# Kernel tuning notes

Measured on AMD Instinct MI355X. Metric: run time of the kernel, lower is better.

Reference implementation:

```python
import jax, jax.numpy as jnp
import numpy as np

B, S, T, V, E, H = 32, 64, 64, 32000, 512, 1024


def setup_inputs() -> dict:
    key = jax.random.key(0)
    ks = jax.random.split(key, 12)
    n = lambda k, shp, s=0.05: jax.random.normal(k, shp, dtype=jnp.float32) * s
    return {
        "src": jax.random.randint(ks[0], (B, S), 0, V, dtype=jnp.int32),
        "tgt": jax.random.randint(ks[1], (B, T), 0, V, dtype=jnp.int32),
        "enc_emb": n(ks[2], (V, E)),
        "dec_emb": n(ks[3], (V, E)),
        "Wih_e": n(ks[4], (E, H)), "bih_e": jnp.zeros((H,), jnp.float32),
        "Whh_e": n(ks[5], (H, H)), "bhh_e": jnp.zeros((H,), jnp.float32),
        "Wih_d": n(ks[6], (E, H)), "bih_d": jnp.zeros((H,), jnp.float32),
        "Whh_d": n(ks[7], (H, H)), "bhh_d": jnp.zeros((H,), jnp.float32),
        "Wout": n(ks[8], (H, V)), "bout": jnp.zeros((V,), jnp.float32),
    }


def reference(src, tgt, enc_emb, dec_emb, Wih_e, bih_e, Whh_e, bhh_e,
              Wih_d, bih_d, Whh_d, bhh_d, Wout, bout):
    # Embedding lookups: [B, S, E] / [B, T, E]
    src_e = enc_emb[src]
    tgt_e = dec_emb[tgt]
    # Precompute input-to-hidden projections for every timestep (same math,
    # batched into one GEMM each): [B, S, H] / [B, T, H]
    x_e = jnp.einsum('bse,eh->bsh', src_e, Wih_e) + bih_e
    x_d = jnp.einsum('bte,eh->bth', tgt_e, Wih_d) + bih_d

    h0 = jnp.zeros((src.shape[0], Whh_e.shape[0]), dtype=x_e.dtype)

    def enc_step(h, x):  # h,x: [B, H]
        h = jnp.tanh(x + h @ Whh_e + bhh_e)
        return h, None

    h_enc, _ = jax.lax.scan(enc_step, h0, jnp.swapaxes(x_e, 0, 1))

    def dec_step(h, x):
        h = jnp.tanh(x + h @ Whh_d + bhh_d)
        return h, h

    _, hs = jax.lax.scan(dec_step, h_enc, jnp.swapaxes(x_d, 0, 1))  # [T, B, H]

    logits = jnp.einsum('tbh,hv->tbv', hs, Wout) + bout  # [T, B, V]
    out = jax.nn.log_softmax(logits, axis=-1)
    return jnp.swapaxes(out, 0, 1)  # [B, T, V]
```

## Files before the change

### kernel.cpp

```cpp
#include <hip/hip_runtime.h>
#include <hip/hip_bf16.h>
#include <math.h>

#define B_ 32
#define S_ 64
#define T_ 64
#define V_ 32000
#define E_ 512
#define H_ 1024

typedef __attribute__((ext_vector_type(8))) short short8;
typedef __attribute__((ext_vector_type(4))) float f32x4;

static __device__ __forceinline__ unsigned short f2bf(float f) {
  union { float f; unsigned u; } c; c.f = f;
  unsigned r = (c.u + 0x7fffu + ((c.u >> 16) & 1u)) >> 16;
  return (unsigned short)r;
}

__global__ __launch_bounds__(256)
void dgemm_embed(const int* __restrict__ idx, const float* __restrict__ emb,
                 const float* __restrict__ B, const float* __restrict__ bias,
                 float* __restrict__ C, int M, int N, int K) {
  __shared__ float As[32][68];
  __shared__ float Bs[32][64];
  const int nbm = M >> 6;
  const int bm = blockIdx.x % nbm;
  const int bn = blockIdx.x / nbm;
  const int tid = threadIdx.x;
  const int tr = tid >> 4, tc = tid & 15;

  const int arow = tid >> 3, acol = (tid & 7) * 4;
  const float* arp[2];
#pragma unroll
  for (int p = 0; p < 2; ++p) {
    int r = arow + p * 32;
    arp[p] = emb + (size_t)idx[bm * 64 + r] * E_;
  }

  double acc[4][4] = {};

  for (int kt = 0; kt < K; kt += 32) {
    {
#pragma unroll
      for (int p = 0; p < 2; ++p) {
        int r = arow + p * 32;
        float4 v = *(const float4*)(arp[p] + kt + acol);
        As[acol + 0][r] = v.x; As[acol + 1][r] = v.y;
        As[acol + 2][r] = v.z; As[acol + 3][r] = v.w;
      }
      int brow = tid >> 4, bcol = (tid & 15) * 4;
#pragma unroll
      for (int p = 0; p < 2; ++p) {
        int r = brow + p * 16;
        float4 v = *(const float4*)(B + (size_t)(kt + r) * N + bn * 64 + bcol);
        *(float4*)(&Bs[r][bcol]) = v;
      }
    }
    __syncthreads();
#pragma unroll
    for (int k = 0; k < 32; ++k) {
      float4 av = *(const float4*)(&As[k][tr * 4]);
      float4 bv = *(const float4*)(&Bs[k][tc * 4]);
      double a[4] = {(double)av.x, (double)av.y, (double)av.z, (double)av.w};
      double b[4] = {(double)bv.x, (double)bv.y, (double)bv.z, (double)bv.w};
#pragma unroll
      for (int i = 0; i < 4; ++i)
#pragma unroll
        for (int j = 0; j < 4; ++j) acc[i][j] = fma(a[i], b[j], acc[i][j]);
    }
    __syncthreads();
  }
#pragma unroll
  for (int i = 0; i < 4; ++i) {
    int gm = bm * 64 + tr * 4 + i;
    int gn = bn * 64 + tc * 4;
    float4 o;
    o.x = (float)(acc[i][0] + (double)bias[gn + 0]);
    o.y = (float)(acc[i][1] + (double)bias[gn + 1]);
    o.z = (float)(acc[i][2] + (double)bias[gn + 2]);
    o.w = (float)(acc[i][3] + (double)bias[gn + 3]);
    *(float4*)(C + (size_t)gm * N + gn) = o;
  }
}

__global__ __launch_bounds__(256)
void transpose_f32(const float* __restrict__ W, float* __restrict__ WT,
                   int K, int N) {
  __shared__ float t[64][65];
  int k0 = blockIdx.x * 64;
  int n0 = blockIdx.y * 64;
  int tid = threadIdx.x;
  int r = tid >> 4, c4 = tid & 15;
#pragma unroll
  for (int i = 0; i < 4; ++i) {
    int row = r + i * 16;
    float4 v = *(const float4*)(W + (size_t)(k0 + row) * N + n0 + c4 * 4);
    t[row][c4 * 4 + 0] = v.x; t[row][c4 * 4 + 1] = v.y;
    t[row][c4 * 4 + 2] = v.z; t[row][c4 * 4 + 3] = v.w;
  }
  __syncthreads();
#pragma unroll
  for (int i = 0; i < 4; ++i) {
    int n = r + i * 16;
    float4 o;
    o.x = t[c4 * 4 + 0][n]; o.y = t[c4 * 4 + 1][n];
    o.z = t[c4 * 4 + 2][n]; o.w = t[c4 * 4 + 3][n];
    *(float4*)(WT + (size_t)(n0 + n) * K + k0 + c4 * 4) = o;
  }
}

__global__ __launch_bounds__(256)
void transpose_bf16(const float* __restrict__ W, unsigned short* __restrict__ WT,
                    int K, int N) {
  __shared__ float t[64][65];
  int k0 = blockIdx.x * 64;
  int n0 = blockIdx.y * 64;
  int tid = threadIdx.x;
  int r = tid >> 4, c4 = tid & 15;
#pragma unroll
  for (int i = 0; i < 4; ++i) {
    int row = r + i * 16;
    float4 v = *(const float4*)(W + (size_t)(k0 + row) * N + n0 + c4 * 4);
    t[row][c4 * 4 + 0] = v.x; t[row][c4 * 4 + 1] = v.y;
    t[row][c4 * 4 + 2] = v.z; t[row][c4 * 4 + 3] = v.w;
  }
  __syncthreads();
#pragma unroll
  for (int i = 0; i < 4; ++i) {
    int n = r + i * 16;
    ushort4 o;
    o.x = f2bf(t[c4 * 4 + 0][n]); o.y = f2bf(t[c4 * 4 + 1][n]);
    o.z = f2bf(t[c4 * 4 + 2][n]); o.w = f2bf(t[c4 * 4 + 3][n]);
    *(ushort4*)(WT + (size_t)(n0 + n) * K + k0 + c4 * 4) = o;
  }
}

__global__ __launch_bounds__(256)
void gemm_bt_swap(const unsigned short* __restrict__ A, const unsigned short* __restrict__ BT,
                  const float* __restrict__ bias, float* __restrict__ C,
                  int M, int N, int K) {
  __shared__ unsigned short As[128 * 64];
  __shared__ unsigned short Bs[128 * 64];
  const int nbm = M >> 7;
  int idx = blockIdx.x;
  const int cpx = gridDim.x >> 3;
  idx = (idx & 7) * cpx + (idx >> 3);
  const int bm = idx % nbm;
  const int bn = idx / nbm;
  const int tid = threadIdx.x;
  const int lane = tid & 63;
  const int wr = (tid >> 6) >> 1;
  const int wc = (tid >> 6) & 1;

  f32x4 acc[4][4] = {};

  int srow[4], scol8[4], ssw[4];
#pragma unroll
  for (int i = 0; i < 4; ++i) {
    int c = i * 256 + tid;
    srow[i] = c >> 3; scol8[i] = c & 7;
    ssw[i] = scol8[i] ^ (srow[i] & 7);
  }

  short8 av[4], bv[4];
#pragma unroll
  for (int i = 0; i < 4; ++i) {
    av[i] = *(const short8*)(A + (size_t)(bm * 128 + srow[i]) * K + scol8[i] * 8);
    bv[i] = *(const short8*)(BT + (size_t)(bn * 128 + srow[i]) * K + scol8[i] * 8);
  }

  for (int kt = 0; kt < K; kt += 64) {
#pragma unroll
    for (int i = 0; i < 4; ++i) {
      *(short8*)(As + srow[i] * 64 + ssw[i] * 8) = av[i];
      *(short8*)(Bs + srow[i] * 64 + ssw[i] * 8) = bv[i];
    }
    __syncthreads();

    if (kt + 64 < K) {
#pragma unroll
      for (int i = 0; i < 4; ++i) {
        av[i] = *(const short8*)(A + (size_t)(bm * 128 + srow[i]) * K + kt + 64 + scol8[i] * 8);
        bv[i] = *(const short8*)(BT + (size_t)(bn * 128 + srow[i]) * K + kt + 64 + scol8[i] * 8);
      }
    }

#pragma unroll
    for (int kk = 0; kk < 64; kk += 32) {
      int kc = (kk + ((lane >> 4) << 3)) >> 3;
      short8 af[4], bfr[4];
#pragma unroll
      for (int mi = 0; mi < 4; ++mi) {
        int row = wr * 64 + mi * 16 + (lane & 15);
        af[mi] = *(const short8*)(As + row * 64 + ((kc ^ (row & 7)) << 3));
      }
#pragma unroll
      for (int ni = 0; ni < 4; ++ni) {
        int row = wc * 64 + ni * 16 + (lane & 15);
        bfr[ni] = *(const short8*)(Bs + row * 64 + ((kc ^ (row & 7)) << 3));
      }
#pragma unroll
      for (int mi = 0; mi < 4; ++mi)
#pragma unroll
        for (int ni = 0; ni < 4; ++ni)
          acc[mi][ni] = __builtin_amdgcn_mfma_f32_16x16x32_bf16(
              af[mi], bfr[ni], acc[mi][ni], 0, 0, 0);
    }
    __syncthreads();
  }

  const int cq = (lane >> 4) << 2;
  const int cn = lane & 15;
#pragma unroll
  for (int mi = 0; mi < 4; ++mi) {
#pragma unroll
    for (int ni = 0; ni < 4; ++ni) {
      int gn = bn * 128 + wc * 64 + ni * 16 + cn;
      float bvv = bias[gn];
#pragma unroll
      for (int q = 0; q < 4; ++q) {
        int gm = bm * 128 + wr * 64 + mi * 16 + cq + q;
        int b = gm & (B_ - 1);
        int t = gm >> 5;
        __builtin_nontemporal_store(acc[mi][ni][q] + bvv,
                                    &C[((size_t)b * T_ + t) * N + gn]);
      }
    }
  }
}

__global__ __launch_bounds__(512)
void rnn_scan_grp2(const float* __restrict__ xe, const float* __restrict__ xd,
                   const float* __restrict__ WTe, const float* __restrict__ WTd,
                   const float* __restrict__ bhhE, const float* __restrict__ bhhD,
                   float* __restrict__ hA, float* __restrict__ hB,
                   unsigned short* __restrict__ hsb, unsigned* __restrict__ bar) {
  __shared__ float hl[4 * 1024];
  const int tid = threadIdx.x;
  const int grp = blockIdx.x & 7;
  const int jslot = blockIdx.x >> 3;
  const int jbase = jslot * 32;
  const int bg = grp * 4;
  const int w = tid >> 6;
  const int l = tid & 63;
  unsigned* mybar = bar + grp * 32;

  const int a = 8 * (l & 1) + 4 * ((l >> 1) & 1) + 2 * ((l >> 2) & 1) +
                ((l >> 3) & 1);
  const int lb = a >> 2;
  const int gb = bg + lb;
  const int gj = jbase + w * 4 + (a & 3);
  const float bje = bhhE[gj];
  const float bjd = bhhD[gj];

  float4 wreg[4][4];
  {
    const float* wsrc = WTe + (size_t)(jbase + w * 4) * 1024;
#pragma unroll
    for (int i = 0; i < 4; ++i) {
      int g = l + 64 * i;
#pragma unroll
      for (int ji = 0; ji < 4; ++ji)
        wreg[i][ji] = *(const float4*)(wsrc + (size_t)ji * 1024 + g * 4);
    }
  }

  for (int t = 0; t < 128; ++t) {
    if (t == 64) {
      const float* wsrc = WTd + (size_t)(jbase + w * 4) * 1024;
#pragma unroll
      for (int i = 0; i < 4; ++i) {
        int g = l + 64 * i;
#pragma unroll
        for (int ji = 0; ji < 4; ++ji)
          wreg[i][ji] = *(const float4*)(wsrc + (size_t)ji * 1024 + g * 4);
      }
    }
    const bool enc = (t < 64);
    const int s = t & 63;
    const float* __restrict__ h_in = (t & 1) ? hB : hA;
    float* __restrict__ h_out = (t & 1) ? hA : hB;
    const float* __restrict__ x = enc ? xe : xd;

    float xv = x[((size_t)gb * 64 + s) * H_ + gj];

    {
      const float* hsrc = h_in + bg * H_;
      float v[8];
#pragma unroll
      for (int u = 0; u < 8; ++u)
        v[u] = __hip_atomic_load(hsrc + u * 512 + tid, __ATOMIC_RELAXED,
                                 __HIP_MEMORY_SCOPE_AGENT);
#pragma unroll
      for (int u = 0; u < 8; ++u)
        hl[u * 512 + tid] = v[u];
    }
    __syncthreads();

    double acc[4][4];
#pragma unroll
    for (int bi = 0; bi < 4; ++bi)
#pragma unroll
      for (int ji = 0; ji < 4; ++ji) acc[bi][ji] = 0.;

#pragma unroll
    for (int i = 0; i < 4; ++i) {
      int g = l + 64 * i;
      float4 hv[4];
#pragma unroll
      for (int bi = 0; bi < 4; ++bi)
        hv[bi] = *(const float4*)(hl + bi * 1024 + g * 4);
#pragma unroll
      for (int bi = 0; bi < 4; ++bi)
#pragma unroll
        for (int ji = 0; ji < 4; ++ji) {
          acc[bi][ji] = fma((double)hv[bi].x, (double)wreg[i][ji].x, acc[bi][ji]);
          acc[bi][ji] = fma((double)hv[bi].y, (double)wreg[i][ji].y, acc[bi][ji]);
          acc[bi][ji] = fma((double)hv[bi].z, (double)wreg[i][ji].z, acc[bi][ji]);
          acc[bi][ji] = fma((double)hv[bi].w, (double)wreg[i][ji].w, acc[bi][ji]);
        }
    }

    double r8[8], r4[4], r2[2], r1;
#pragma unroll
    for (int aa = 0; aa < 8; ++aa) {
      double send = (l & 1) ? acc[aa >> 2][aa & 3] : acc[(aa + 8) >> 2][(aa + 8) & 3];
      double mine = (l & 1) ? acc[(aa + 8) >> 2][(aa + 8) & 3] : acc[aa >> 2][aa & 3];
      r8[aa] = mine + __shfl_xor(send, 1);
    }
#pragma unroll
    for (int aa = 0; aa < 4; ++aa) {
      double send = (l & 2) ? r8[aa] : r8[aa + 4];
      double mine = (l & 2) ? r8[aa + 4] : r8[aa];
      r4[aa] = mine + __shfl_xor(send, 2);
    }
#pragma unroll
    for (int aa = 0; aa < 2; ++aa) {
      double send = (l & 4) ? r4[aa] : r4[aa + 2];
      double mine = (l & 4) ? r4[aa + 2] : r4[aa];
      r2[aa] = mine + __shfl_xor(send, 4);
    }
    {
      double send = (l & 8) ? r2[0] : r2[1];
      double mine = (l & 8) ? r2[1] : r2[0];
      r1 = mine + __shfl_xor(send, 8);
    }
    r1 += __shfl_xor(r1, 16);
    r1 += __shfl_xor(r1, 32);

    float hf = 0.f;
    if (l < 16) {
      double v = r1 + (double)xv + (double)(enc ? bje : bjd);
      double h = tanh(v);
      hf = (float)h;
      __hip_atomic_store(&h_out[(size_t)gb * H_ + gj], hf, __ATOMIC_RELAXED,
                         __HIP_MEMORY_SCOPE_AGENT);
    }

    if (t < 127) {
      asm volatile("s_waitcnt vmcnt(0)" ::: "memory");
      __syncthreads();
      if (tid == 0) {
        __hip_atomic_fetch_add(mybar, 1u, __ATOMIC_RELAXED,
                               __HIP_MEMORY_SCOPE_AGENT);
        unsigned tgt = 32u * (unsigned)(t + 1);
        while (__hip_atomic_load(mybar, __ATOMIC_RELAXED,
                                 __HIP_MEMORY_SCOPE_AGENT) < tgt)
          __builtin_amdgcn_s_sleep(1);
      }
      __syncthreads();
    }
    if (!enc && l < 16)
      __builtin_nontemporal_store(f2bf(hf),
                                  &hsb[(size_t)s * (B_ * H_) + (size_t)gb * H_ + gj]);
  }
}

__global__ __launch_bounds__(1024)
void log_softmax_rows(float* __restrict__ out) {
  __shared__ float rl[32000];
  __shared__ float wm[16], wsv[16];
  float* row = out + (size_t)blockIdx.x * V_;
  const int tid = threadIdx.x;
  float m = -INFINITY, s = 0.f;
  for (int i = tid; i < V_ / 4; i += 1024) {
    float4 v = *(const float4*)(row + i * 4);
    *(float4*)(rl + i * 4) = v;
    float mx = fmaxf(fmaxf(v.x, v.y), fmaxf(v.z, v.w));
    if (mx > m) { s *= __expf(m - mx); m = mx; }
    s += __expf(v.x - m) + __expf(v.y - m) + __expf(v.z - m) + __expf(v.w - m);
  }
#pragma unroll
  for (int o = 32; o; o >>= 1) {
    float mo = __shfl_xor(m, o);
    float so = __shfl_xor(s, o);
    float mn = fmaxf(m, mo);
    s = s * __expf(m - mn) + so * __expf(mo - mn);
    m = mn;
  }
  int wv = tid >> 6;
  if ((tid & 63) == 0) { wm[wv] = m; wsv[wv] = s; }
  __syncthreads();
  float M = wm[0];
#pragma unroll
  for (int i = 1; i < 16; ++i) M = fmaxf(M, wm[i]);
  float Ssum = 0.f;
#pragma unroll
  for (int i = 0; i < 16; ++i) Ssum += wsv[i] * __expf(wm[i] - M);
  float L = M + logf(Ssum);
  for (int i = tid; i < V_ / 4; i += 1024) {
    float4 v = *(const float4*)(rl + i * 4);
    v.x -= L; v.y -= L; v.z -= L; v.w -= L;
    __builtin_nontemporal_store(v.x, &row[i * 4 + 0]);
    __builtin_nontemporal_store(v.y, &row[i * 4 + 1]);
    __builtin_nontemporal_store(v.z, &row[i * 4 + 2]);
    __builtin_nontemporal_store(v.w, &row[i * 4 + 3]);
  }
}

extern "C" void kernel_launch(void* const* d_in, const int* in_sizes, int n_in,
                              void* d_out, int out_size, void* d_ws, size_t ws_size,
                              hipStream_t stream) {
  const int*   src  = (const int*)  d_in[0];
  const int*   tgt  = (const int*)  d_in[1];
  const float* encE = (const float*)d_in[2];
  const float* decE = (const float*)d_in[3];
  const float* WihE = (const float*)d_in[4];
  const float* bihE = (const float*)d_in[5];
  const float* WhhE = (const float*)d_in[6];
  const float* bhhE = (const float*)d_in[7];
  const float* WihD = (const float*)d_in[8];
  const float* bihD = (const float*)d_in[9];
  const float* WhhD = (const float*)d_in[10];
  const float* bhhD = (const float*)d_in[11];
  const float* Wout = (const float*)d_in[12];
  const float* bout = (const float*)d_in[13];
  float* out = (float*)d_out;

  char* w = (char*)d_ws;
  float* x_e = (float*)w;                      w += (size_t)2048 * 1024 * 4;
  float* x_d = (float*)w;                      w += (size_t)2048 * 1024 * 4;
  float* h0  = (float*)w;                      w += 32 * 1024 * 4;
  float* h1  = (float*)w;                      w += 32 * 1024 * 4;
  unsigned* bar = (unsigned*)w;                w += 8 * 32 * 4;
  float* WhhTe = (float*)w;                    w += (size_t)1024 * 1024 * 4;
  float* WhhTd = (float*)w;                    w += (size_t)1024 * 1024 * 4;
  unsigned short* hsb   = (unsigned short*)w;  w += (size_t)2048 * 1024 * 2;
  unsigned short* WoutT = (unsigned short*)w;  w += (size_t)V_ * 1024 * 2;

  dgemm_embed<<<(2048 / 64) * (H_ / 64), 256, 0, stream>>>(src, encE, WihE, bihE,
                                                           x_e, 2048, H_, E_);
  dgemm_embed<<<(2048 / 64) * (H_ / 64), 256, 0, stream>>>(tgt, decE, WihD, bihD,
                                                           x_d, 2048, H_, E_);

  transpose_f32<<<dim3(H_ / 64, H_ / 64), 256, 0, stream>>>(WhhE, WhhTe, H_, H_);
  transpose_f32<<<dim3(H_ / 64, H_ / 64), 256, 0, stream>>>(WhhD, WhhTd, H_, H_);

  hipMemsetAsync(h0, 0, 32 * 1024 * 4, stream);
  hipMemsetAsync(bar, 0, 8 * 32 * 4, stream);
  rnn_scan_grp2<<<256, 512, 0, stream>>>(x_e, x_d, WhhTe, WhhTd, bhhE, bhhD,
                                         h0, h1, hsb, bar);

  transpose_bf16<<<dim3(H_ / 64, V_ / 64), 256, 0, stream>>>(Wout, WoutT, H_, V_);
  gemm_bt_swap<<<(2048 / 128) * (V_ / 128), 256, 0, stream>>>(hsb, WoutT, bout, out,
                                                              2048, V_, H_);
  log_softmax_rows<<<B_ * T_, 1024, 0, stream>>>(out);
}
```

Measured before the change: 1.022 ms.

## Merge paired launches and stage output GEMM epilogue through LDS for coalesced stores

The two embedding GEMMs and the two recurrent-weight transposes are each merged into a single launch that picks its operand set from the block index, removing launch overhead and filling more CUs. The output GEMM epilogue now writes accumulators into shared memory reusing the A/B tile buffers, then reads them back so each thread stores four contiguous floats per row. This replaces the scattered per-element stores. It adds extra barriers and LDS traffic in the epilogue.

```diff
diff --git a/kernel.cpp b/kernel.cpp
--- a/kernel.cpp
+++ b/kernel.cpp
@@ -19,14 +19,25 @@
 }
 
 __global__ __launch_bounds__(256)
-void dgemm_embed(const int* __restrict__ idx, const float* __restrict__ emb,
-                 const float* __restrict__ B, const float* __restrict__ bias,
-                 float* __restrict__ C, int M, int N, int K) {
+void dgemm_embed_dual(const int* __restrict__ idx0, const float* __restrict__ emb0,
+                      const float* __restrict__ B0, const float* __restrict__ bias0,
+                      float* __restrict__ C0,
+                      const int* __restrict__ idx1, const float* __restrict__ emb1,
+                      const float* __restrict__ B1, const float* __restrict__ bias1,
+                      float* __restrict__ C1, int M, int N, int K) {
+  const int half = blockIdx.x >> 9;
+  const int bid = blockIdx.x & 511;
+  const int* __restrict__ idx = half ? idx1 : idx0;
+  const float* __restrict__ emb = half ? emb1 : emb0;
+  const float* __restrict__ B = half ? B1 : B0;
+  const float* __restrict__ bias = half ? bias1 : bias0;
+  float* __restrict__ C = half ? C1 : C0;
+
   __shared__ float As[32][68];
   __shared__ float Bs[32][64];
   const int nbm = M >> 6;
-  const int bm = blockIdx.x % nbm;
-  const int bn = blockIdx.x / nbm;
+  const int bm = bid % nbm;
+  const int bn = bid / nbm;
   const int tid = threadIdx.x;
   const int tr = tid >> 4, tc = tid & 15;
 
@@ -85,11 +96,16 @@
 }
 
 __global__ __launch_bounds__(256)
-void transpose_f32(const float* __restrict__ W, float* __restrict__ WT,
-                   int K, int N) {
+void transpose_f32_dual(const float* __restrict__ W0, float* __restrict__ WT0,
+                        const float* __restrict__ W1, float* __restrict__ WT1,
+                        int K, int N) {
+  const int half = blockIdx.y >> 4;
+  const int by = blockIdx.y & 15;
+  const float* __restrict__ W = half ? W1 : W0;
+  float* __restrict__ WT = half ? WT1 : WT0;
   __shared__ float t[64][65];
   int k0 = blockIdx.x * 64;
-  int n0 = blockIdx.y * 64;
+  int n0 = by * 64;
   int tid = threadIdx.x;
   int r = tid >> 4, c4 = tid & 15;
 #pragma unroll
@@ -140,8 +156,9 @@
 void gemm_bt_swap(const unsigned short* __restrict__ A, const unsigned short* __restrict__ BT,
                   const float* __restrict__ bias, float* __restrict__ C,
                   int M, int N, int K) {
-  __shared__ unsigned short As[128 * 64];
-  __shared__ unsigned short Bs[128 * 64];
+  __shared__ unsigned short AsBs[2][128 * 64];
+  unsigned short* As = AsBs[0];
+  unsigned short* Bs = AsBs[1];
   const int nbm = M >> 7;
   int idx = blockIdx.x;
   const int cpx = gridDim.x >> 3;
@@ -210,22 +227,35 @@
     __syncthreads();
   }
 
+  float* Ct = (float*)AsBs;
   const int cq = (lane >> 4) << 2;
   const int cn = lane & 15;
 #pragma unroll
   for (int mi = 0; mi < 4; ++mi) {
+    if (mi) __syncthreads();
 #pragma unroll
     for (int ni = 0; ni < 4; ++ni) {
       int gn = bn * 128 + wc * 64 + ni * 16 + cn;
       float bvv = bias[gn];
 #pragma unroll
-      for (int q = 0; q < 4; ++q) {
-        int gm = bm * 128 + wr * 64 + mi * 16 + cq + q;
-        int b = gm & (B_ - 1);
-        int t = gm >> 5;
-        __builtin_nontemporal_store(acc[mi][ni][q] + bvv,
-                                    &C[((size_t)b * T_ + t) * N + gn]);
-      }
+      for (int q = 0; q < 4; ++q)
+        Ct[(wr * 16 + cq + q) * 132 + wc * 64 + ni * 16 + cn] =
+            acc[mi][ni][q] + bvv;
+    }
+    __syncthreads();
+#pragma unroll
+    for (int p = 0; p < 4; ++p) {
+      int f = p * 256 + tid;
+      int r = f >> 5, c4 = f & 31;
+      float4 v = *(const float4*)(Ct + r * 132 + c4 * 4);
+      int gm = bm * 128 + (r >> 4) * 64 + mi * 16 + (r & 15);
+      int b = gm & (B_ - 1);
+      int t = gm >> 5;
+      float* dstp = &C[((size_t)b * T_ + t) * N + bn * 128 + c4 * 4];
+      __builtin_nontemporal_store(v.x, dstp + 0);
+      __builtin_nontemporal_store(v.y, dstp + 1);
+      __builtin_nontemporal_store(v.z, dstp + 2);
+      __builtin_nontemporal_store(v.w, dstp + 3);
     }
   }
 }
@@ -449,13 +479,12 @@
   unsigned short* hsb   = (unsigned short*)w;  w += (size_t)2048 * 1024 * 2;
   unsigned short* WoutT = (unsigned short*)w;  w += (size_t)V_ * 1024 * 2;
 
-  dgemm_embed<<<(2048 / 64) * (H_ / 64), 256, 0, stream>>>(src, encE, WihE, bihE,
-                                                           x_e, 2048, H_, E_);
-  dgemm_embed<<<(2048 / 64) * (H_ / 64), 256, 0, stream>>>(tgt, decE, WihD, bihD,
-                                                           x_d, 2048, H_, E_);
-
-  transpose_f32<<<dim3(H_ / 64, H_ / 64), 256, 0, stream>>>(WhhE, WhhTe, H_, H_);
-  transpose_f32<<<dim3(H_ / 64, H_ / 64), 256, 0, stream>>>(WhhD, WhhTd, H_, H_);
+  dgemm_embed_dual<<<1024, 256, 0, stream>>>(src, encE, WihE, bihE, x_e,
+                                             tgt, decE, WihD, bihD, x_d,
+                                             2048, H_, E_);
+
+  transpose_f32_dual<<<dim3(H_ / 64, 2 * (H_ / 64)), 256, 0, stream>>>(
+      WhhE, WhhTe, WhhD, WhhTd, H_, H_);
 
   hipMemsetAsync(h0, 0, 32 * 1024 * 4, stream);
   hipMemsetAsync(bar, 0, 8 * 32 * 4, stream);
```

Measured after the change: 973.7 us. 1.05x faster.
